# Optimization experiments

Measured on AMD Instinct MI355X. Metric: run time of the kernel, lower is better.

The kernel has to match this reference:

```python
import jax, jax.numpy as jnp
import numpy as np

N_IN = 512
N_OUT = 256
T = 2048
B = 32


def setup_inputs() -> dict:
    key = jax.random.key(0)
    ks = jax.random.split(key, 9)
    s_in = 1.0 / np.sqrt(N_IN)
    inp = {
        "xt": jax.random.normal(ks[0], (T, B, N_IN), dtype=jnp.float32),
        "ct_forward": jax.random.normal(ks[1], (1, B, N_OUT), dtype=jnp.float32),
        # weights stored torch-style as [out, in]
        "Wx": jax.random.uniform(ks[2], (N_OUT, N_IN), jnp.float32, -s_in, s_in),
        "Wf": jax.random.uniform(ks[3], (N_OUT, N_IN), jnp.float32, -s_in, s_in),
        "bf": jax.random.uniform(ks[4], (N_OUT,), jnp.float32, -s_in, s_in),
        "Wr": jax.random.uniform(ks[5], (N_OUT, N_IN), jnp.float32, -s_in, s_in),
        "br": jax.random.uniform(ks[6], (N_OUT,), jnp.float32, -s_in, s_in),
        "Wc": jax.random.uniform(ks[7], (N_OUT, N_IN), jnp.float32, -s_in, s_in),
        "bc": jax.random.uniform(ks[8], (N_OUT,), jnp.float32, -s_in, s_in),
    }
    return inp


def reference(xt, ct_forward, Wx, Wf, bf, Wr, br, Wc, bc):
    # Batched projections over all timesteps (the GEMM part of SRU).
    x_proj = jnp.einsum("tbi,oi->tbo", xt, Wx)              # [T,B,n_out]
    f = jax.nn.sigmoid(jnp.einsum("tbi,oi->tbo", xt, Wf) + bf)
    r = jax.nn.sigmoid(jnp.einsum("tbi,oi->tbo", xt, Wr) + br)
    cx = jnp.einsum("tbi,oi->tbo", xt, Wc) + bc

    def step(c, inp):
        x_t, ft, rt, cxt = inp
        c = ft * c + (1.0 - ft) * x_t
        h = rt * jnp.tanh(c) + (1.0 - rt) * cxt
        return c, h

    c_final, ht = jax.lax.scan(step, ct_forward[0], (x_proj, f, r, cx))
    # dropout=0.0 -> identity; forward returns (ht, ct)
    return ht, c_final
```

## Files before the change

kernel.cpp:

```cpp
#include <hip/hip_runtime.h>
#include <stdint.h>

#define T_STEPS 2048
#define BATCH   32
#define NIN     512
#define NOUT    256
#define MROWS   (T_STEPS*BATCH)
#define BO      (BATCH*NOUT)
#define NCHUNK  32
#define CHLEN   (T_STEPS/NCHUNK)

typedef _Float16 f16x8 __attribute__((ext_vector_type(8)));
typedef _Float16 f16x4 __attribute__((ext_vector_type(4)));
typedef float    fx4   __attribute__((ext_vector_type(4)));

#define LDSP(p) ((__attribute__((address_space(3))) void*)(p))
#define GLBP(p) ((const __attribute__((address_space(1))) void*)(p))

#define BAR()        asm volatile("s_barrier" ::: "memory")
#define DRAIN_LGKM() asm volatile("s_waitcnt lgkmcnt(0)" ::: "memory")
#define WAITVM(n)    do { asm volatile("s_waitcnt vmcnt(" #n ")" ::: "memory"); __builtin_amdgcn_sched_barrier(0); } while(0)

__global__ __launch_bounds__(256) void convert_x(
    const float* __restrict__ xt, _Float16* __restrict__ xh)
{
    long i = ((long)blockIdx.x * 256 + threadIdx.x) * 8;
    float4 v0 = *(const float4*)(xt + i);
    float4 v1 = *(const float4*)(xt + i + 4);
    f16x8 h;
    h[0] = (_Float16)v0.x; h[1] = (_Float16)v0.y;
    h[2] = (_Float16)v0.z; h[3] = (_Float16)v0.w;
    h[4] = (_Float16)v1.x; h[5] = (_Float16)v1.y;
    h[6] = (_Float16)v1.z; h[7] = (_Float16)v1.w;
    *(f16x8*)(xh + i) = h;
}

__global__ __launch_bounds__(256) void convert_w(
    const float* __restrict__ Wx, const float* __restrict__ Wf,
    const float* __restrict__ Wr, const float* __restrict__ Wc,
    _Float16* __restrict__ Wcat)
{
    int idx = blockIdx.x * 256 + threadIdx.x;
    int n  = idx >> 7;
    int k4 = (idx & 127) * 4;
    int g = n >> 8, o = n & 255;
    const float* W = (g == 0) ? Wx : (g == 1) ? Wf : (g == 2) ? Wr : Wc;
    float4 v = *(const float4*)(W + o * NIN + k4);
    f16x4 h;
    h[0] = (_Float16)v.x; h[1] = (_Float16)v.y;
    h[2] = (_Float16)v.z; h[3] = (_Float16)v.w;
    *(f16x4*)(Wcat + n * NIN + k4) = h;
}

#define BM 256
#define BN 256
#define BK 64
#define NGT 32

__global__ __launch_bounds__(512, 2) void gemm_proj(
    const _Float16* __restrict__ xh,
    const _Float16* __restrict__ Wcat,
    const float* __restrict__ bfv, const float* __restrict__ brv, const float* __restrict__ bcv,
    _Float16* __restrict__ xp_h, _Float16* __restrict__ f_h,
    _Float16* __restrict__ r_h,  _Float16* __restrict__ cx_h)
{
    __shared__ char lds[131072];

    const int tid  = threadIdx.x;
    const int lane = tid & 63;
    const int w    = tid >> 6;
    const int wrq  = w >> 2;
    const int wcq  = w & 3;
    const int lr = lane & 15, lk = lane >> 4;

    int wg = (blockIdx.x & 7) * 32 + (blockIdx.x >> 3);
    const int  cg   = wg & 3;
    const int  mgrp = wg >> 2;
    const long m0 = (long)mgrp * 1024;
    const int  n0 = cg * BN;

    const int rl8  = lane >> 3;
    const int scol = (((lane & 7) ^ rl8) << 4);
    const char* baseA = (const char*)xh   + (m0 + w * 8 + rl8) * 1024 + scol;
    const char* baseB = (const char*)Wcat + ((long)(n0 + w * 8 + rl8)) * 1024 + scol;

#define STAGE_A(g, h) do {                                                   \
        char* _d = lds + ((g) & 1) * 32768 + (h) * 16384 + w * 1024;         \
        const char* _s = baseA + (long)((g) >> 3) * 262144                   \
                         + ((g) & 7) * 128 + (long)(h) * 131072;             \
        __builtin_amdgcn_global_load_lds(GLBP(_s),         LDSP(_d),        16, 0, 0); \
        __builtin_amdgcn_global_load_lds(GLBP(_s + 65536), LDSP(_d + 8192), 16, 0, 0); \
    } while (0)
#define STAGE_B(g, h) do {                                                   \
        char* _d = lds + 65536 + ((g) & 1) * 32768 + (h) * 16384 + w * 1024; \
        const char* _s = baseB + ((g) & 7) * 128 + (long)(h) * 131072;       \
        __builtin_amdgcn_global_load_lds(GLBP(_s),         LDSP(_d),        16, 0, 0); \
        __builtin_amdgcn_global_load_lds(GLBP(_s + 65536), LDSP(_d + 8192), 16, 0, 0); \
    } while (0)

    fx4 acc[2][2][4][2];
    #pragma unroll
    for (int a = 0; a < 2; ++a)
        #pragma unroll
        for (int b = 0; b < 2; ++b)
            #pragma unroll
            for (int c = 0; c < 4; ++c)
                #pragma unroll
                for (int d = 0; d < 2; ++d)
                    acc[a][b][c][d] = (fx4){0.f, 0.f, 0.f, 0.f};

    f16x8 Ar0[4][2];
    f16x8 Ar1[4][2];
    f16x8 B0r[2][2];
    f16x8 B1r[2][2];

#define READ_A(c2, h, dst) do {                                              \
        _Pragma("unroll")                                                    \
        for (int mf = 0; mf < 4; ++mf) {                                     \
            int rl = wrq * 64 + mf * 16 + lr;                                \
            int rb = (c2) * 32768 + (h) * 16384 + rl * 128;                  \
            _Pragma("unroll")                                                \
            for (int kk = 0; kk < 2; ++kk)                                   \
                dst[mf][kk] = *(const f16x8*)(lds + rb +                     \
                    ((kk * 64 + lk * 16) ^ ((rl & 7) << 4)));                \
        }                                                                    \
    } while (0)
#define READ_B(c2, h, dst) do {                                              \
        _Pragma("unroll")                                                    \
        for (int nf = 0; nf < 2; ++nf) {                                     \
            int rl = wcq * 32 + nf * 16 + lr;                                \
            int rb = 65536 + (c2) * 32768 + (h) * 16384 + rl * 128;          \
            _Pragma("unroll")                                                \
            for (int kk = 0; kk < 2; ++kk)                                   \
                dst[nf][kk] = *(const f16x8*)(lds + rb +                     \
                    ((kk * 64 + lk * 16) ^ ((rl & 7) << 4)));                \
        }                                                                    \
    } while (0)
#define MMACC(Qr, Qc, Aa, Br) do {                                           \
        _Pragma("unroll")                                                    \
        for (int kk = 0; kk < 2; ++kk)                                       \
            _Pragma("unroll")                                                \
            for (int mf = 0; mf < 4; ++mf)                                   \
                _Pragma("unroll")                                            \
                for (int nf = 0; nf < 2; ++nf)                               \
                    acc[Qr][Qc][mf][nf] = __builtin_amdgcn_mfma_f32_16x16x32_f16( \
                        Br[nf][kk], Aa[mf][kk], acc[Qr][Qc][mf][nf], 0, 0, 0);    \
    } while (0)

    const int g_out = cg;
    _Float16* outp = (g_out == 0) ? xp_h : (g_out == 1) ? f_h : (g_out == 2) ? r_h : cx_h;
    const float* bias = (g_out == 1) ? bfv : (g_out == 2) ? brv : (g_out == 3) ? bcv : nullptr;

    STAGE_A(0, 0); STAGE_B(0, 0); STAGE_B(0, 1); STAGE_A(0, 1);
    STAGE_A(1, 0); STAGE_B(1, 0);
    WAITVM(4);
    BAR();

    for (int g = 0; g < NGT; ++g) {
        const int c2 = g & 1;
        READ_A(c2, 0, Ar0);
        READ_B(c2, 0, B0r);
        DRAIN_LGKM();
        BAR();
        if (g + 1 < NGT) { STAGE_B(g + 1, 1); STAGE_A(g + 1, 1); }
        if (g + 2 < NGT) { STAGE_A(g + 2, 0); STAGE_B(g + 2, 0); }
        READ_B(c2, 1, B1r);
        READ_A(c2, 1, Ar1);
        MMACC(0, 0, Ar0, B0r);
        MMACC(0, 1, Ar0, B1r);
        MMACC(1, 0, Ar1, B0r);
        MMACC(1, 1, Ar1, B1r);
        if (g < NGT - 2)       WAITVM(4);
        else if (g == NGT - 2) WAITVM(0);
        BAR();
        if ((g & 7) == 7) {
            const long mbase = m0 + (long)(g >> 3) * 256;
            #pragma unroll
            for (int Qr = 0; Qr < 2; ++Qr) {
                #pragma unroll
                for (int Qc = 0; Qc < 2; ++Qc) {
                    #pragma unroll
                    for (int nf = 0; nf < 2; ++nf) {
                        const int ob = Qc * 128 + wcq * 32 + nf * 16 + lk * 4;
                        float4 bv4 = (g_out == 0) ? (float4){0.f, 0.f, 0.f, 0.f}
                                                  : *(const float4*)(bias + ob);
                        #pragma unroll
                        for (int mf = 0; mf < 4; ++mf) {
                            long row = mbase + Qr * 128 + wrq * 64 + mf * 16 + lr;
                            fx4 v = acc[Qr][Qc][mf][nf];
                            f16x4 hv;
                            if (g_out == 1 || g_out == 2) {
                                float p0 = v[0] + bv4.x, p1 = v[1] + bv4.y;
                                float p2 = v[2] + bv4.z, p3 = v[3] + bv4.w;
                                hv[0] = (_Float16)(__builtin_amdgcn_rcpf(1.0f + __expf(-p0)));
                                hv[1] = (_Float16)(__builtin_amdgcn_rcpf(1.0f + __expf(-p1)));
                                hv[2] = (_Float16)(__builtin_amdgcn_rcpf(1.0f + __expf(-p2)));
                                hv[3] = (_Float16)(__builtin_amdgcn_rcpf(1.0f + __expf(-p3)));
                            } else {
                                hv[0] = (_Float16)(v[0] + bv4.x);
                                hv[1] = (_Float16)(v[1] + bv4.y);
                                hv[2] = (_Float16)(v[2] + bv4.z);
                                hv[3] = (_Float16)(v[3] + bv4.w);
                            }
                            *(f16x4*)(outp + row * NOUT + ob) = hv;
                            acc[Qr][Qc][mf][nf] = (fx4){0.f, 0.f, 0.f, 0.f};
                        }
                    }
                }
            }
        }
    }
}

__global__ __launch_bounds__(256) void chunk_scan_a(
    const _Float16* __restrict__ f_h, const _Float16* __restrict__ xp_h,
    float* __restrict__ chunkA, float* __restrict__ chunkB)
{
    int tid = blockIdx.x * 256 + threadIdx.x;
    int chunk = tid >> 13;
    int bo = tid & (BO - 1);
    long base = (long)chunk * CHLEN * BO + bo;
    float a = 1.f, cc = 0.f;
    #pragma unroll 4
    for (int s = 0; s < CHLEN; ++s) {
        long i = base + (long)s * BO;
        float fv = (float)f_h[i];
        float xv = (float)xp_h[i];
        cc = fv * cc + (1.f - fv) * xv;
        a *= fv;
    }
    chunkA[tid] = a;
    chunkB[tid] = cc;
}

__global__ __launch_bounds__(256) void chunk_prop(
    const float* __restrict__ ct0,
    const float* __restrict__ chunkA, const float* __restrict__ chunkB,
    float* __restrict__ cin, float* __restrict__ c_final)
{
    int bo = blockIdx.x * 256 + threadIdx.x;
    float c = ct0[bo];
    #pragma unroll
    for (int ch = 0; ch < NCHUNK; ++ch) {
        cin[ch * BO + bo] = c;
        c = chunkA[ch * BO + bo] * c + chunkB[ch * BO + bo];
    }
    c_final[bo] = c;
}

__global__ __launch_bounds__(256) void chunk_scan_h(
    const _Float16* __restrict__ xp_h, const _Float16* __restrict__ f_h,
    const _Float16* __restrict__ r_h,  const _Float16* __restrict__ cx_h,
    const float* __restrict__ cin, float* __restrict__ ht)
{
    int tid = blockIdx.x * 256 + threadIdx.x;
    int chunk = tid >> 13;
    int bo = tid & (BO - 1);
    long base = (long)chunk * CHLEN * BO + bo;
    float c = cin[tid];
    #pragma unroll 4
    for (int s = 0; s < CHLEN; ++s) {
        long i = base + (long)s * BO;
        float fv = (float)f_h[i];
        float xv = (float)xp_h[i];
        float rv = (float)r_h[i];
        float cxv = (float)cx_h[i];
        c = fv * c + (1.f - fv) * xv;
        float e = __expf(2.f * c);
        float th = (e - 1.f) * __builtin_amdgcn_rcpf(e + 1.f);
        ht[i] = rv * th + (1.f - rv) * cxv;
    }
}

extern "C" void kernel_launch(void* const* d_in, const int* in_sizes, int n_in,
                              void* d_out, int out_size, void* d_ws, size_t ws_size,
                              hipStream_t stream) {
    const float* xt  = (const float*)d_in[0];
    const float* ct0 = (const float*)d_in[1];
    const float* Wx  = (const float*)d_in[2];
    const float* Wf  = (const float*)d_in[3];
    const float* bf_ = (const float*)d_in[4];
    const float* Wr  = (const float*)d_in[5];
    const float* br_ = (const float*)d_in[6];
    const float* Wc  = (const float*)d_in[7];
    const float* bc_ = (const float*)d_in[8];

    float* ht      = (float*)d_out;
    float* c_final = ht + (size_t)MROWS * NOUT;

    char* ws = (char*)d_ws;
    _Float16* Wcat = (_Float16*)ws;
    _Float16* xh   = (_Float16*)(ws + (1 << 20));
    _Float16* xp_h = xh + (size_t)MROWS * NIN;
    _Float16* f_h  = xp_h + (size_t)MROWS * NOUT;
    _Float16* r_h  = f_h  + (size_t)MROWS * NOUT;
    _Float16* cx_h = r_h  + (size_t)MROWS * NOUT;
    float* chunkA  = (float*)(cx_h + (size_t)MROWS * NOUT);
    float* chunkB  = chunkA + NCHUNK * BO;
    float* cin     = chunkB + NCHUNK * BO;

    convert_w<<<512, 256, 0, stream>>>(Wx, Wf, Wr, Wc, Wcat);
    convert_x<<<(MROWS * NIN / 8) / 256, 256, 0, stream>>>(xt, xh);
    gemm_proj<<<256, 512, 0, stream>>>(
        xh, Wcat, bf_, br_, bc_, xp_h, f_h, r_h, cx_h);
    chunk_scan_a<<<(NCHUNK * BO) / 256, 256, 0, stream>>>(f_h, xp_h, chunkA, chunkB);
    chunk_prop<<<BO / 256, 256, 0, stream>>>(ct0, chunkA, chunkB, cin, c_final);
    chunk_scan_h<<<(NCHUNK * BO) / 256, 256, 0, stream>>>(xp_h, f_h, r_h, cx_h, cin, ht);
}
```

Before: 192.1 us.

## Fuse fp32-to-fp16 x conversion into GEMM A-load and vectorize chunk scans

Drops the separate convert_x kernel. The GEMM now loads fp32 x tiles through registers and converts them to fp16 before storing to LDS, which removes a full fp16 copy of x written to and re-read from global memory. The GEMM pipeline changes from asynchronous global_load_lds double staging to register-staged loads with full vmcnt drains each iteration, so load/compute overlap is reduced. The chunk scan kernels now handle four outputs per thread with vector loads, which cuts their launch size to 256 blocks and may lower occupancy and latency hiding.

```diff
diff --git a/kernel.cpp b/kernel.cpp
--- a/kernel.cpp
+++ b/kernel.cpp
@@ -20,20 +20,6 @@
 #define BAR()        asm volatile("s_barrier" ::: "memory")
 #define DRAIN_LGKM() asm volatile("s_waitcnt lgkmcnt(0)" ::: "memory")
 #define WAITVM(n)    do { asm volatile("s_waitcnt vmcnt(" #n ")" ::: "memory"); __builtin_amdgcn_sched_barrier(0); } while(0)
-
-__global__ __launch_bounds__(256) void convert_x(
-    const float* __restrict__ xt, _Float16* __restrict__ xh)
-{
-    long i = ((long)blockIdx.x * 256 + threadIdx.x) * 8;
-    float4 v0 = *(const float4*)(xt + i);
-    float4 v1 = *(const float4*)(xt + i + 4);
-    f16x8 h;
-    h[0] = (_Float16)v0.x; h[1] = (_Float16)v0.y;
-    h[2] = (_Float16)v0.z; h[3] = (_Float16)v0.w;
-    h[4] = (_Float16)v1.x; h[5] = (_Float16)v1.y;
-    h[6] = (_Float16)v1.z; h[7] = (_Float16)v1.w;
-    *(f16x8*)(xh + i) = h;
-}
 
 __global__ __launch_bounds__(256) void convert_w(
     const float* __restrict__ Wx, const float* __restrict__ Wf,
@@ -58,7 +44,7 @@
 #define NGT 32
 
 __global__ __launch_bounds__(512, 2) void gemm_proj(
-    const _Float16* __restrict__ xh,
+    const float*    __restrict__ xt,
     const _Float16* __restrict__ Wcat,
     const float* __restrict__ bfv, const float* __restrict__ brv, const float* __restrict__ bcv,
     _Float16* __restrict__ xp_h, _Float16* __restrict__ f_h,
@@ -79,17 +65,29 @@
     const long m0 = (long)mgrp * 1024;
     const int  n0 = cg * BN;
 
+    const char* baseAg = (const char*)xt + (m0 + (tid >> 4)) * 2048 + (tid & 15) * 16;
+    const int awb = (tid >> 4) * 128 + (((tid & 15) * 8) ^ (((tid >> 4) & 7) << 4));
+
     const int rl8  = lane >> 3;
     const int scol = (((lane & 7) ^ rl8) << 4);
-    const char* baseA = (const char*)xh   + (m0 + w * 8 + rl8) * 1024 + scol;
     const char* baseB = (const char*)Wcat + ((long)(n0 + w * 8 + rl8)) * 1024 + scol;
 
-#define STAGE_A(g, h) do {                                                   \
-        char* _d = lds + ((g) & 1) * 32768 + (h) * 16384 + w * 1024;         \
-        const char* _s = baseA + (long)((g) >> 3) * 262144                   \
-                         + ((g) & 7) * 128 + (long)(h) * 131072;             \
-        __builtin_amdgcn_global_load_lds(GLBP(_s),         LDSP(_d),        16, 0, 0); \
-        __builtin_amdgcn_global_load_lds(GLBP(_s + 65536), LDSP(_d + 8192), 16, 0, 0); \
+    float4 av[8];
+#define ALOAD(g) do {                                                        \
+        const char* _b = baseAg + (long)((g) >> 3) * 524288 + ((g) & 7) * 256; \
+        _Pragma("unroll")                                                    \
+        for (int j = 0; j < 8; ++j)                                          \
+            av[j] = *(const float4*)(_b + j * 65536);                        \
+    } while (0)
+#define AWRITE(g) do {                                                       \
+        char* _d = lds + ((g) & 1) * 32768 + awb;                            \
+        _Pragma("unroll")                                                    \
+        for (int j = 0; j < 8; ++j) {                                        \
+            f16x4 _h;                                                        \
+            _h[0] = (_Float16)av[j].x; _h[1] = (_Float16)av[j].y;            \
+            _h[2] = (_Float16)av[j].z; _h[3] = (_Float16)av[j].w;            \
+            *(f16x4*)(_d + j * 4096) = _h;                                   \
+        }                                                                    \
     } while (0)
 #define STAGE_B(g, h) do {                                                   \
         char* _d = lds + 65536 + ((g) & 1) * 32768 + (h) * 16384 + w * 1024; \
@@ -109,10 +107,8 @@
                 for (int d = 0; d < 2; ++d)
                     acc[a][b][c][d] = (fx4){0.f, 0.f, 0.f, 0.f};
 
-    f16x8 Ar0[4][2];
-    f16x8 Ar1[4][2];
-    f16x8 B0r[2][2];
-    f16x8 B1r[2][2];
+    f16x8 Ar0[4][2], Ar1[4][2];
+    f16x8 B0r[2][2], B1r[2][2];
 
 #define READ_A(c2, h, dst) do {                                              \
         _Pragma("unroll")                                                    \
@@ -151,27 +147,34 @@
     _Float16* outp = (g_out == 0) ? xp_h : (g_out == 1) ? f_h : (g_out == 2) ? r_h : cx_h;
     const float* bias = (g_out == 1) ? bfv : (g_out == 2) ? brv : (g_out == 3) ? bcv : nullptr;
 
-    STAGE_A(0, 0); STAGE_B(0, 0); STAGE_B(0, 1); STAGE_A(0, 1);
-    STAGE_A(1, 0); STAGE_B(1, 0);
-    WAITVM(4);
+    ALOAD(0);
+    WAITVM(0);
+    AWRITE(0);
+    STAGE_B(0, 0); STAGE_B(0, 1);
+    WAITVM(0);
+    DRAIN_LGKM();
     BAR();
 
     for (int g = 0; g < NGT; ++g) {
         const int c2 = g & 1;
         READ_A(c2, 0, Ar0);
         READ_B(c2, 0, B0r);
-        DRAIN_LGKM();
-        BAR();
-        if (g + 1 < NGT) { STAGE_B(g + 1, 1); STAGE_A(g + 1, 1); }
-        if (g + 2 < NGT) { STAGE_A(g + 2, 0); STAGE_B(g + 2, 0); }
         READ_B(c2, 1, B1r);
         READ_A(c2, 1, Ar1);
+        if (g + 1 < NGT) {
+            ALOAD(g + 1);
+            STAGE_B(g + 1, 0); STAGE_B(g + 1, 1);
+        }
         MMACC(0, 0, Ar0, B0r);
         MMACC(0, 1, Ar0, B1r);
         MMACC(1, 0, Ar1, B0r);
         MMACC(1, 1, Ar1, B1r);
-        if (g < NGT - 2)       WAITVM(4);
-        else if (g == NGT - 2) WAITVM(0);
+        if (g + 1 < NGT) {
+            WAITVM(4);
+            AWRITE(g + 1);
+            WAITVM(0);
+        }
+        DRAIN_LGKM();
         BAR();
         if ((g & 7) == 7) {
             const long mbase = m0 + (long)(g >> 3) * 256;
@@ -216,21 +219,25 @@
     const _Float16* __restrict__ f_h, const _Float16* __restrict__ xp_h,
     float* __restrict__ chunkA, float* __restrict__ chunkB)
 {
-    int tid = blockIdx.x * 256 + threadIdx.x;
-    int chunk = tid >> 13;
-    int bo = tid & (BO - 1);
-    long base = (long)chunk * CHLEN * BO + bo;
-    float a = 1.f, cc = 0.f;
-    #pragma unroll 4
+    int tid2 = blockIdx.x * 256 + threadIdx.x;
+    int ch = tid2 >> 11;
+    int b4 = (tid2 & 2047) << 2;
+    long base = (long)ch * CHLEN * BO + b4;
+    fx4 a = (fx4){1.f, 1.f, 1.f, 1.f};
+    fx4 cc = (fx4){0.f, 0.f, 0.f, 0.f};
     for (int s = 0; s < CHLEN; ++s) {
         long i = base + (long)s * BO;
-        float fv = (float)f_h[i];
-        float xv = (float)xp_h[i];
-        cc = fv * cc + (1.f - fv) * xv;
-        a *= fv;
+        f16x4 fv = *(const f16x4*)(f_h + i);
+        f16x4 xv = *(const f16x4*)(xp_h + i);
+        #pragma unroll
+        for (int q = 0; q < 4; ++q) {
+            float f = (float)fv[q], x = (float)xv[q];
+            cc[q] = f * cc[q] + (1.f - f) * x;
+            a[q] *= f;
+        }
     }
-    chunkA[tid] = a;
-    chunkB[tid] = cc;
+    *(fx4*)(chunkA + ch * BO + b4) = a;
+    *(fx4*)(chunkB + ch * BO + b4) = cc;
 }
 
 __global__ __launch_bounds__(256) void chunk_prop(
@@ -253,22 +260,28 @@
     const _Float16* __restrict__ r_h,  const _Float16* __restrict__ cx_h,
     const float* __restrict__ cin, float* __restrict__ ht)
 {
-    int tid = blockIdx.x * 256 + threadIdx.x;
-    int chunk = tid >> 13;
-    int bo = tid & (BO - 1);
-    long base = (long)chunk * CHLEN * BO + bo;
-    float c = cin[tid];
-    #pragma unroll 4
+    int tid2 = blockIdx.x * 256 + threadIdx.x;
+    int ch = tid2 >> 11;
+    int b4 = (tid2 & 2047) << 2;
+    long base = (long)ch * CHLEN * BO + b4;
+    fx4 c = *(const fx4*)(cin + ch * BO + b4);
     for (int s = 0; s < CHLEN; ++s) {
         long i = base + (long)s * BO;
-        float fv = (float)f_h[i];
-        float xv = (float)xp_h[i];
-        float rv = (float)r_h[i];
-        float cxv = (float)cx_h[i];
-        c = fv * c + (1.f - fv) * xv;
-        float e = __expf(2.f * c);
-        float th = (e - 1.f) * __builtin_amdgcn_rcpf(e + 1.f);
-        ht[i] = rv * th + (1.f - rv) * cxv;
+        f16x4 fv  = *(const f16x4*)(f_h + i);
+        f16x4 xv  = *(const f16x4*)(xp_h + i);
+        f16x4 rv  = *(const f16x4*)(r_h + i);
+        f16x4 cxv = *(const f16x4*)(cx_h + i);
+        fx4 h4;
+        #pragma unroll
+        for (int q = 0; q < 4; ++q) {
+            float f = (float)fv[q], x = (float)xv[q];
+            float r = (float)rv[q], cx = (float)cxv[q];
+            c[q] = f * c[q] + (1.f - f) * x;
+            float e = __expf(2.f * c[q]);
+            float th = (e - 1.f) * __builtin_amdgcn_rcpf(e + 1.f);
+            h4[q] = r * th + (1.f - r) * cx;
+        }
+        *(fx4*)(ht + i) = h4;
     }
 }
 
@@ -290,8 +303,7 @@
 
     char* ws = (char*)d_ws;
     _Float16* Wcat = (_Float16*)ws;
-    _Float16* xh   = (_Float16*)(ws + (1 << 20));
-    _Float16* xp_h = xh + (size_t)MROWS * NIN;
+    _Float16* xp_h = (_Float16*)(ws + (1 << 20));
     _Float16* f_h  = xp_h + (size_t)MROWS * NOUT;
     _Float16* r_h  = f_h  + (size_t)MROWS * NOUT;
     _Float16* cx_h = r_h  + (size_t)MROWS * NOUT;
@@ -300,10 +312,9 @@
     float* cin     = chunkB + NCHUNK * BO;
 
     convert_w<<<512, 256, 0, stream>>>(Wx, Wf, Wr, Wc, Wcat);
-    convert_x<<<(MROWS * NIN / 8) / 256, 256, 0, stream>>>(xt, xh);
     gemm_proj<<<256, 512, 0, stream>>>(
-        xh, Wcat, bf_, br_, bc_, xp_h, f_h, r_h, cx_h);
-    chunk_scan_a<<<(NCHUNK * BO) / 256, 256, 0, stream>>>(f_h, xp_h, chunkA, chunkB);
+        xt, Wcat, bf_, br_, bc_, xp_h, f_h, r_h, cx_h);
+    chunk_scan_a<<<256, 256, 0, stream>>>(f_h, xp_h, chunkA, chunkB);
     chunk_prop<<<BO / 256, 256, 0, stream>>>(ct0, chunkA, chunkB, cin, c_final);
-    chunk_scan_h<<<(NCHUNK * BO) / 256, 256, 0, stream>>>(xp_h, f_h, r_h, cx_h, cin, ht);
-}
+    chunk_scan_h<<<256, 256, 0, stream>>>(xp_h, f_h, r_h, cx_h, cin, ht);
+}
```

Result: slower. 323.5 us (+68.4%).
